# Kernel optimization log

Measured on AMD Instinct MI355X. Metric: run time of the kernel, lower is better.

Reference implementation:

```python
import jax, jax.numpy as jnp
import numpy as np

B, C, H, W = 8, 384, 32, 32
KEYS, HEADS, U = 16, 4, 1
VS = C // HEADS
N = H * W
BN_EPS = 1e-5


def setup_inputs() -> dict:
    key = jax.random.key(0)
    ks = jax.random.split(key, 8)
    x = jax.random.normal(ks[0], (B, C, H, W), dtype=jnp.float32)
    # 1x1 convs (spectral-normalized in torch; SN only rescales the weight,
    # so a plain weight matrix computes the same functional form)
    Wq = jax.random.normal(ks[1], (KEYS * HEADS, C), dtype=jnp.float32) * 0.02
    Wk = jax.random.normal(ks[2], (KEYS * U, C), dtype=jnp.float32) * 0.02
    Wv = jax.random.normal(ks[3], (VS * U, C), dtype=jnp.float32) * 0.02
    # BatchNorm affine params (torch code xavier-inits weight, zeros bias)
    gamma_q = jax.random.normal(ks[4], (KEYS * HEADS,), dtype=jnp.float32)
    beta_q = jnp.zeros((KEYS * HEADS,), dtype=jnp.float32)
    gamma_v = jax.random.normal(ks[5], (VS * U,), dtype=jnp.float32)
    beta_v = jnp.zeros((VS * U,), dtype=jnp.float32)
    pos_emb = jax.random.normal(ks[6], (N, N, KEYS, U), dtype=jnp.float32)
    return {"x": x, "Wq": Wq, "Wk": Wk, "Wv": Wv,
            "gamma_q": gamma_q, "beta_q": beta_q,
            "gamma_v": gamma_v, "beta_v": beta_v,
            "pos_emb": pos_emb}


def _bn(z, gamma, beta):
    # z: (B, Ch, N); BatchNorm2d in training mode: biased batch stats over (B, N)
    mean = jnp.mean(z, axis=(0, 2), keepdims=True)
    var = jnp.var(z, axis=(0, 2), keepdims=True)
    zn = (z - mean) * jax.lax.rsqrt(var + BN_EPS)
    return zn * gamma[None, :, None] + beta[None, :, None]


def reference(x, Wq, Wk, Wv, gamma_q, beta_q, gamma_v, beta_v, pos_emb):
    xf = x.reshape(B, C, N)                       # 1x1 conv == per-pixel matmul
    q = jnp.einsum('oc,bcn->bon', Wq, xf)         # (B, KEYS*HEADS, N)
    k = jnp.einsum('oc,bcn->bon', Wk, xf)         # (B, KEYS*U, N)
    v = jnp.einsum('oc,bcn->bon', Wv, xf)         # (B, VS*U, N)
    q = _bn(q, gamma_q, beta_q)
    v = _bn(v, gamma_v, beta_v)
    q = q.reshape(B, HEADS, KEYS, N)
    k = k.reshape(B, U, KEYS, N)
    v = v.reshape(B, U, VS, N)
    k = jax.nn.softmax(k, axis=-1)
    lambdac = jnp.einsum('bukm,buvm->bkv', k, v)          # content lambda
    Yc = jnp.einsum('bhkn,bkv->bhvn', q, lambdac)
    lambdap = jnp.einsum('nmku,buvm->bnkv', pos_emb, v)   # position lambda (B,N,K,V)
    Yp = jnp.einsum('bhkn,bnkv->bhvn', q, lambdap)
    Y = (Yc + Yp).reshape(B, C, H, W)
    return Y
```

## Files before the change

### kernel.cpp

```cpp
#include <hip/hip_runtime.h>

typedef __attribute__((ext_vector_type(8))) short short8;
typedef __attribute__((ext_vector_type(16))) float floatx16;
typedef __attribute__((ext_vector_type(4))) float floatx4;
typedef unsigned short ushort16_t;
typedef unsigned int uint32;

#define BB 8
#define CC 384
#define NPIX 1024
#define TOTCH 176
#define BN_EPS 1e-5f

__device__ __forceinline__ ushort16_t f2bf(float x) {
    uint32 u = __float_as_uint(x);
    u += 0x7FFFu + ((u >> 16) & 1u);
    return (ushort16_t)(u >> 16);
}
__device__ __forceinline__ uint32 pk2(float a, float b) {
    uint32 ua = __float_as_uint(a); ua += 0x7FFFu + ((ua >> 16) & 1u);
    uint32 ub = __float_as_uint(b); ub += 0x7FFFu + ((ub >> 16) & 1u);
    return (ua >> 16) | (ub & 0xFFFF0000u);
}
__device__ __forceinline__ void dma16(const ushort16_t* g, ushort16_t* l) {
    __builtin_amdgcn_global_load_lds(
        (const __attribute__((address_space(1))) uint32*)g,
        (__attribute__((address_space(3))) uint32*)l, 16, 0, 0);
}
__device__ __forceinline__ int div48(int x) {
    return (int)(((unsigned)x * 21846u) >> 20);
}


__global__ __launch_bounds__(256) void k_xt(const float* __restrict__ x,
    const float* __restrict__ Wq, const float* __restrict__ Wk,
    const float* __restrict__ Wv,
    ushort16_t* __restrict__ xbf, ushort16_t* __restrict__ wbf)
{
    int bx = blockIdx.x, t = threadIdx.x;
    if (bx < 256) {
        __shared__ __align__(16) ushort16_t T[32 * 392];
        int col0 = bx * 32;
        int b = col0 >> 10, nbase = col0 & 1023;
        const float* xb = x + (size_t)b * (CC * NPIX) + nbase;
        #pragma unroll
        for (int j = 0; j < 12; ++j) {
            int idx = t + 256 * j;
            int c = idx >> 3, ng = idx & 7;
            float4 f = *(const float4*)(xb + (size_t)c * NPIX + ng * 4);
            int n = ng * 4;
            T[(n + 0) * 392 + c] = f2bf(f.x);
            T[(n + 1) * 392 + c] = f2bf(f.y);
            T[(n + 2) * 392 + c] = f2bf(f.z);
            T[(n + 3) * 392 + c] = f2bf(f.w);
        }
        __syncthreads();
        #pragma unroll
        for (int j = 0; j < 6; ++j) {
            int task = t + 256 * j;
            int col = div48(task);
            int ch  = task - col * 48;
            uint4 w = *(const uint4*)&T[col * 392 + ch * 8];
            *(uint4*)&xbf[(size_t)(col0 + col) * CC + ch * 8] = w;
        }
    } else {
        #pragma unroll
        for (int jj = 0; jj < 9; ++jj) {
            int idx8 = ((bx - 256) * 9 + jj) * 256 + t;
            int row = div48(idx8);
            int g   = idx8 - row * 48;
            float4 f0, f1;
            if (row < 176) {
                const float* src;
                if (row < 64)       src = Wq + (size_t)row * CC;
                else if (row < 80)  src = Wk + (size_t)(row - 64) * CC;
                else                src = Wv + (size_t)(row - 80) * CC;
                f0 = *(const float4*)(src + g * 8);
                f1 = *(const float4*)(src + g * 8 + 4);
            } else {
                f0.x = f0.y = f0.z = f0.w = 0.f;
                f1 = f0;
            }
            uint4 w;
            w.x = pk2(f0.x, f0.y); w.y = pk2(f0.z, f0.w);
            w.z = pk2(f1.x, f1.y); w.w = pk2(f1.z, f1.w);
            *(uint4*)&wbf[(size_t)row * CC + g * 8] = w;
        }
    }
}

__global__ __launch_bounds__(256) void k_proj(const ushort16_t* __restrict__ xbf,
    const ushort16_t* __restrict__ wbf, float* __restrict__ qkv)
{
    int t = threadIdx.x;
    int wave = t >> 6, lane = t & 63;
    int ct = blockIdx.x * 4 + wave;
    int r0 = blockIdx.y * 16;
    int col = ct * 16 + (lane & 15);
    int kh  = lane >> 4;
    const ushort16_t* ap = wbf + (size_t)(r0 + (lane & 15)) * CC + kh * 8;
    const ushort16_t* bp = xbf + (size_t)col * CC + kh * 8;
    floatx4 acc = {0.f, 0.f, 0.f, 0.f};
    short8 a0 = *(const short8*)ap;
    short8 b0 = *(const short8*)bp;
    #pragma unroll
    for (int k = 1; k < 12; ++k) {
        short8 a1 = *(const short8*)(ap + k * 32);
        short8 b1 = *(const short8*)(bp + k * 32);
        acc = __builtin_amdgcn_mfma_f32_16x16x32_bf16(a0, b0, acc, 0, 0, 0);
        a0 = a1; b0 = b1;
    }
    acc = __builtin_amdgcn_mfma_f32_16x16x32_bf16(a0, b0, acc, 0, 0, 0);
    int b = col >> 10, n = col & 1023;
    #pragma unroll
    for (int r = 0; r < 4; ++r) {
        int ch = r0 + (lane >> 4) * 4 + r;
        qkv[((size_t)b * TOTCH + ch) * NPIX + n] = acc[r];
    }
}

__global__ __launch_bounds__(256) void k_bnsm(const float* __restrict__ qkv,
    const float* __restrict__ gq, const float* __restrict__ bq,
    const float* __restrict__ gv, const float* __restrict__ bv,
    float* __restrict__ sA, float* __restrict__ sB, float* __restrict__ ksm)
{
    int bx = blockIdx.x, tid = threadIdx.x;
    int wid = tid >> 6, lane = tid & 63;
    if (bx < 160) {
        int ch = bx;
        int row; float gamma, beta;
        if (ch < 64) { row = ch; gamma = gq[ch]; beta = bq[ch]; }
        else { int j = ch - 64; row = 80 + j; gamma = gv[j]; beta = bv[j]; }
        float s = 0.f, ss = 0.f;
        #pragma unroll
        for (int j = 0; j < 8; ++j) {
            int i4 = tid + 256 * j;
            int b = i4 >> 8, n4 = i4 & 255;
            float4 f = *(const float4*)(qkv + ((size_t)b * TOTCH + row) * NPIX
                                            + n4 * 4);
            s  += f.x + f.y + f.z + f.w;
            ss += f.x * f.x + f.y * f.y + f.z * f.z + f.w * f.w;
        }
        #pragma unroll
        for (int off = 32; off > 0; off >>= 1) {
            s  += __shfl_down(s, off);
            ss += __shfl_down(ss, off);
        }
        __shared__ float rs[4], rss[4];
        if (lane == 0) { rs[wid] = s; rss[wid] = ss; }
        __syncthreads();
        if (tid == 0) {
            float S  = rs[0] + rs[1] + rs[2] + rs[3];
            float SS = rss[0] + rss[1] + rss[2] + rss[3];
            float inv = 1.f / (BB * NPIX);
            float mean = S * inv;
            float var  = SS * inv - mean * mean;
            float a = gamma * rsqrtf(var + BN_EPS);
            sA[row] = a;
            sB[row] = beta - mean * a;
        }
    } else {
        int idx = bx - 160;
        int kc = idx & 15, b = idx >> 4;
        const float* rowp = qkv + ((size_t)b * TOTCH + 64 + kc) * NPIX;
        float4 v4 = *(const float4*)(rowp + tid * 4);
        float v[4] = {v4.x, v4.y, v4.z, v4.w};
        float mx = fmaxf(fmaxf(v[0], v[1]), fmaxf(v[2], v[3]));
        #pragma unroll
        for (int off = 32; off > 0; off >>= 1) mx = fmaxf(mx, __shfl_down(mx, off));
        __shared__ float sm[4], ssum[4];
        if (lane == 0) sm[wid] = mx;
        __syncthreads();
        mx = fmaxf(fmaxf(sm[0], sm[1]), fmaxf(sm[2], sm[3]));
        float e[4], s = 0.f;
        #pragma unroll
        for (int j = 0; j < 4; ++j) { e[j] = __expf(v[j] - mx); s += e[j]; }
        #pragma unroll
        for (int off = 32; off > 0; off >>= 1) s += __shfl_down(s, off);
        if (lane == 0) ssum[wid] = s;
        __syncthreads();
        float inv = 1.f / (ssum[0] + ssum[1] + ssum[2] + ssum[3]);
        float4 o;
        o.x = e[0] * inv; o.y = e[1] * inv; o.z = e[2] * inv; o.w = e[3] * inv;
        *(float4*)(ksm + ((size_t)b * 16 + kc) * NPIX + tid * 4) = o;
    }
}

__global__ __launch_bounds__(256) void k_packlc(const float* __restrict__ qkv,
    const float* __restrict__ sA, const float* __restrict__ sB,
    const float* __restrict__ ksm,
    ushort16_t* __restrict__ qt_g, ushort16_t* __restrict__ vt_g,
    ushort16_t* __restrict__ lc_g)
{
    int bx = blockIdx.x, t = threadIdx.x;
    if (bx < 128) {
        int bh = t & 31, nn = (t >> 5) & 7;
        int n = bx * 8 + nn;
        int b = bh >> 2, h = bh & 3;
        float vals[16];
        #pragma unroll
        for (int k = 0; k < 16; ++k) {
            int ch = h * 16 + k;
            vals[k] = qkv[((size_t)b * TOTCH + ch) * NPIX + n] * sA[ch] + sB[ch];
        }
        uint4 w0, w1;
        w0.x = pk2(vals[0], vals[1]);  w0.y = pk2(vals[2], vals[3]);
        w0.z = pk2(vals[4], vals[5]);  w0.w = pk2(vals[6], vals[7]);
        w1.x = pk2(vals[8], vals[9]);  w1.y = pk2(vals[10], vals[11]);
        w1.z = pk2(vals[12], vals[13]); w1.w = pk2(vals[14], vals[15]);
        *(uint4*)&qt_g[(size_t)n * 512 + bh * 8]       = w0;
        *(uint4*)&qt_g[(size_t)n * 512 + 256 + bh * 8] = w1;
    } else if (bx < 512) {
        int gi = (bx - 128) * 256 + t;
        int m8 = gi & 127;
        int vg = (gi >> 7) % 96;
        int b  = gi / (96 * 128);
        int m  = m8 * 8;
        int row = 80 + vg;
        float a = sA[row], bb = sB[row];
        const float* p = qkv + ((size_t)b * TOTCH + row) * NPIX + m;
        float4 f0 = *(const float4*)p;
        float4 f1 = *(const float4*)(p + 4);
        uint4 w;
        w.x = pk2(f0.x * a + bb, f0.y * a + bb);
        w.y = pk2(f0.z * a + bb, f0.w * a + bb);
        w.z = pk2(f1.x * a + bb, f1.y * a + bb);
        w.w = pk2(f1.z * a + bb, f1.w * a + bb);
        int mt = m >> 5, mq = (m >> 3) & 3;
        int vhh = vg / 48, vtt = (vg % 48) >> 4, vl = vg & 15;
        size_t idx = ((((size_t)b * 32 + mt) * 2 + vhh) * 3 + vtt) * 512
                   + mq * 128 + vl * 8;
        *(uint4*)&vt_g[idx] = w;
    } else {
        int gi = bx - 512;
        int v = gi % 96, b = gi / 96;
        int row = 80 + v;
        float a = sA[row], bb = sB[row];
        const float* vp = qkv + ((size_t)b * TOTCH + row) * NPIX;
        const float* kp = ksm + (size_t)b * 16 * NPIX;
        float acc[16];
        #pragma unroll
        for (int k = 0; k < 16; ++k) acc[k] = 0.f;
        for (int m = t; m < NPIX; m += 256) {
            float vv = vp[m] * a + bb;
            #pragma unroll
            for (int k = 0; k < 16; ++k) acc[k] += kp[k * NPIX + m] * vv;
        }
        #pragma unroll
        for (int k = 0; k < 16; ++k) {
            #pragma unroll
            for (int off = 32; off > 0; off >>= 1)
                acc[k] += __shfl_down(acc[k], off);
        }
        __shared__ float red[16][4];
        int wid = t >> 6, lane = t & 63;
        if (lane == 0) {
            #pragma unroll
            for (int k = 0; k < 16; ++k) red[k][wid] = acc[k];
        }
        __syncthreads();
        int vhh = v / 48, vtt = (v % 48) >> 4, vl = v & 15;
        size_t plane = ((size_t)(b * 2 + vhh) * 3 + vtt) * 512;
        if (t < 16) {
            int k = t;
            float val = red[k][0] + red[k][1] + red[k][2] + red[k][3];
            lc_g[plane + (k >> 3) * 128 + vl * 8 + (k & 7)] = f2bf(val);
        } else if (t < 18) {
            int mq = 2 + (t - 16);
            uint4 z; z.x = z.y = z.z = z.w = 0u;
            *(uint4*)&lc_g[plane + mq * 128 + vl * 8] = z;
        }
    }
}

__global__ __launch_bounds__(512, 2) void k_main(const float* __restrict__ pos,
    const ushort16_t* __restrict__ qt_g, const ushort16_t* __restrict__ vt_g,
    const ushort16_t* __restrict__ lc_g, float* __restrict__ out)
{
    __shared__ __align__(16) ushort16_t P_s[8192];
    __shared__ __align__(16) ushort16_t V_s[24576];
    __shared__ __align__(16) ushort16_t S_s[8192];
    int tid  = threadIdx.x;
    int lane = tid & 63;
    int wave = tid >> 6;
    int n0 = blockIdx.x * 8;
    int vh = blockIdx.y;

    int col1 = lane & 31, half = lane >> 5;
    int pb = col1 >> 2, ph = col1 & 3;
    int pplane = pb * 2 + (ph >> 1);
    int pf = pplane & 7;
    int pcb = ph & 1;
    int sm = tid & 31, snn = (tid >> 5) & 7, skh = (tid >> 8) & 1;
    int b2 = wave;

    short8 qfr = *(const short8*)(qt_g + (size_t)(n0 + wave) * 512
                                  + half * 256 + col1 * 8);

    floatx4 acc[2][3];
    #pragma unroll
    for (int hg = 0; hg < 2; ++hg)
        #pragma unroll
        for (int vt = 0; vt < 3; ++vt)
            acc[hg][vt] = floatx4{0.f, 0.f, 0.f, 0.f};

    const float* pbase = pos + ((size_t)(n0 + snn) * 1024 + sm) * 16 + skh * 8;

    {
        float4 f0 = *(const float4*)pbase;
        float4 f1 = *(const float4*)(pbase + 4);
        uint4 w;
        w.x = pk2(f0.x, f0.y); w.y = pk2(f0.z, f0.w);
        w.z = pk2(f1.x, f1.y); w.w = pk2(f1.z, f1.w);
        *(uint4*)&P_s[(snn * 2 + skh) * 256 + sm * 8] = w;
        const ushort16_t* src = vt_g + (size_t)(((b2 * 32) * 2 + vh) * 3) * 512;
        #pragma unroll
        for (int j = 0; j < 3; ++j)
            dma16(src + j * 512 + lane * 8, &V_s[b2 * 1536 + j * 512]);
    }
    __syncthreads();

    for (int it = 0; it < 32; ++it) {
        float4 pf0, pf1;
        if (it < 31) {
            const float* p = pbase + (size_t)(it + 1) * 32 * 16;
            pf0 = *(const float4*)p;
            pf1 = *(const float4*)(p + 4);
        }
        {
            short8 afr = *(const short8*)&P_s[(it & 1) * 4096
                + wave * 512 + half * 256 + col1 * 8];
            floatx16 d;
            #pragma unroll
            for (int i = 0; i < 16; ++i) d[i] = 0.f;
            d = __builtin_amdgcn_mfma_f32_32x32x16_bf16(afr, qfr, d, 0, 0, 0);
            int nx = wave ^ pf;
            #pragma unroll
            for (int q = 0; q < 4; ++q) {
                int c = q * 16 + pcb * 8 + nx;
                uint2 wv;
                wv.x = pk2(d[q * 4 + 0], d[q * 4 + 1]);
                wv.y = pk2(d[q * 4 + 2], d[q * 4 + 3]);
                *(uint2*)&S_s[pplane * 512 + c * 8 + half * 4] = wv;
            }
        }
        __syncthreads();
        if (it < 31) {
            const ushort16_t* src = vt_g
                + (size_t)(((b2 * 32 + it + 1) * 2 + vh) * 3) * 512;
            #pragma unroll
            for (int j = 0; j < 3; ++j)
                dma16(src + j * 512 + lane * 8,
                      &V_s[((it + 1) & 1) * 12288 + b2 * 1536 + j * 512]);
        }
        {
            int vb = (it & 1) * 12288;
            short8 av[3];
            #pragma unroll
            for (int vt = 0; vt < 3; ++vt)
                av[vt] = *(const short8*)&V_s[vb + b2 * 1536 + vt * 512 + lane * 8];
            #pragma unroll
            for (int hg = 0; hg < 2; ++hg) {
                int p2 = b2 * 2 + hg, f2 = p2 & 7;
                short8 bs = *(const short8*)&S_s[p2 * 512
                    + ((lane >> 4) * 16 + ((lane & 15) ^ f2)) * 8];
                #pragma unroll
                for (int vt = 0; vt < 3; ++vt)
                    acc[hg][vt] = __builtin_amdgcn_mfma_f32_16x16x32_bf16(
                        av[vt], bs, acc[hg][vt], 0, 0, 0);
            }
        }
        if (it < 31) {
            uint4 w;
            w.x = pk2(pf0.x, pf0.y); w.y = pk2(pf0.z, pf0.w);
            w.z = pk2(pf1.x, pf1.y); w.w = pk2(pf1.z, pf1.w);
            *(uint4*)&P_s[((it + 1) & 1) * 4096 + (snn * 2 + skh) * 256 + sm * 8] = w;
        }
        __syncthreads();
    }

    {
        const ushort16_t* src = lc_g + (size_t)((b2 * 2 + vh) * 3) * 512;
        #pragma unroll
        for (int j = 0; j < 3; ++j)
            dma16(src + j * 512 + lane * 8, &V_s[b2 * 1536 + j * 512]);
    }
    {
        int c = half * 16 + pcb * 8 + (wave ^ pf);
        *(short8*)&S_s[pplane * 512 + c * 8] = qfr;
        int zp = tid >> 5, zr = tid & 31;
        int zc = (2 + (zr >> 4)) * 16 + ((zr & 15) ^ (zp & 7));
        uint4 z; z.x = z.y = z.z = z.w = 0u;
        *(uint4*)&S_s[zp * 512 + zc * 8] = z;
    }
    __syncthreads();
    {
        short8 av[3];
        #pragma unroll
        for (int vt = 0; vt < 3; ++vt)
            av[vt] = *(const short8*)&V_s[b2 * 1536 + vt * 512 + lane * 8];
        #pragma unroll
        for (int hg = 0; hg < 2; ++hg) {
            int p2 = b2 * 2 + hg, f2 = p2 & 7;
            short8 bs = *(const short8*)&S_s[p2 * 512
                + ((lane >> 4) * 16 + ((lane & 15) ^ f2)) * 8];
            #pragma unroll
            for (int vt = 0; vt < 3; ++vt)
                acc[hg][vt] = __builtin_amdgcn_mfma_f32_16x16x32_bf16(
                    av[vt], bs, acc[hg][vt], 0, 0, 0);
        }
    }

    {
        int cn = lane & 15;
        int nloc = cn & 7;
        #pragma unroll
        for (int hg = 0; hg < 2; ++hg) {
            int h = hg * 2 + (cn >> 3);
            #pragma unroll
            for (int vt = 0; vt < 3; ++vt) {
                #pragma unroll
                for (int r = 0; r < 4; ++r) {
                    int v = vh * 48 + vt * 16 + (lane >> 4) * 4 + r;
                    out[(size_t)(b2 * 384 + h * 96 + v) * 1024 + n0 + nloc]
                        = acc[hg][vt][r];
                }
            }
        }
    }
}

extern "C" void kernel_launch(void* const* d_in, const int* in_sizes, int n_in,
                              void* d_out, int out_size, void* d_ws, size_t ws_size,
                              hipStream_t stream) {
    const float* x   = (const float*)d_in[0];
    const float* Wq  = (const float*)d_in[1];
    const float* Wk  = (const float*)d_in[2];
    const float* Wv  = (const float*)d_in[3];
    const float* gq  = (const float*)d_in[4];
    const float* bq  = (const float*)d_in[5];
    const float* gv  = (const float*)d_in[6];
    const float* bv  = (const float*)d_in[7];
    const float* pos = (const float*)d_in[8];
    float* out = (float*)d_out;
    float* ws  = (float*)d_ws;

    float* qkv = ws;
    float* sA  = ws + 1441792;
    float* sB  = ws + 1441968;
    float* ksm = ws + 1442144;
    ushort16_t* qt_g = (ushort16_t*)(ws + 1573216);
    ushort16_t* vt_g = (ushort16_t*)(ws + 1835360);
    ushort16_t* lc_g = (ushort16_t*)(ws + 2228576);
    ushort16_t* xbf  = (ushort16_t*)(ws + 2240864);
    ushort16_t* wbf  = (ushort16_t*)(ws + 3813728);

    k_xt<<<dim3(260), dim3(256), 0, stream>>>(x, Wq, Wk, Wv, xbf, wbf);
    k_proj<<<dim3(128, 11), dim3(256), 0, stream>>>(xbf, wbf, qkv);
    k_bnsm<<<dim3(288), dim3(256), 0, stream>>>(qkv, gq, bq, gv, bv, sA, sB, ksm);
    k_packlc<<<dim3(1280), dim3(256), 0, stream>>>(qkv, sA, sB, ksm,
                                                   qt_g, vt_g, lc_g);
    k_main<<<dim3(128, 2), dim3(512), 0, stream>>>(pos, qt_g, vt_g, lc_g, out);
}
```

Measured before the change: 184.8 us.

## Load position fragments directly into registers and double-buffer scores to drop a barrier

Each wave now loads its pos_emb rows straight into the MFMA A-operand layout and converts them to bf16 in registers. This removes the P_s shared-memory staging buffer along with its stores and loads. The score tile S_s is double-buffered, so the second __syncthreads in each of the 32 iterations can go, leaving one barrier per step. In exchange, each lane issues its own strided 32-byte global loads and the kernel holds extra prefetch registers, and shared-memory use stays about the same.

```diff
diff --git a/kernel.cpp b/kernel.cpp
--- a/kernel.cpp
+++ b/kernel.cpp
@@ -277,9 +277,8 @@
     const ushort16_t* __restrict__ qt_g, const ushort16_t* __restrict__ vt_g,
     const ushort16_t* __restrict__ lc_g, float* __restrict__ out)
 {
-    __shared__ __align__(16) ushort16_t P_s[8192];
-    __shared__ __align__(16) ushort16_t V_s[24576];
-    __shared__ __align__(16) ushort16_t S_s[8192];
+    __shared__ __align__(16) ushort16_t V_s[2][12288];
+    __shared__ __align__(16) ushort16_t S_s[2][8192];
     int tid  = threadIdx.x;
     int lane = tid & 63;
     int wave = tid >> 6;
@@ -291,7 +290,6 @@
     int pplane = pb * 2 + (ph >> 1);
     int pf = pplane & 7;
     int pcb = ph & 1;
-    int sm = tid & 31, snn = (tid >> 5) & 7, skh = (tid >> 8) & 1;
     int b2 = wave;
 
     short8 qfr = *(const short8*)(qt_g + (size_t)(n0 + wave) * 512
@@ -304,44 +302,44 @@
         for (int vt = 0; vt < 3; ++vt)
             acc[hg][vt] = floatx4{0.f, 0.f, 0.f, 0.f};
 
-    const float* pbase = pos + ((size_t)(n0 + snn) * 1024 + sm) * 16 + skh * 8;
-
+    floatx16 z16;
+    #pragma unroll
+    for (int i = 0; i < 16; ++i) z16[i] = 0.f;
+
+    const float* pA = pos + ((size_t)(n0 + wave) * 1024 + col1) * 16 + half * 8;
+
+    float4 a0 = *(const float4*)pA;
+    float4 a1 = *(const float4*)(pA + 4);
     {
-        float4 f0 = *(const float4*)pbase;
-        float4 f1 = *(const float4*)(pbase + 4);
-        uint4 w;
-        w.x = pk2(f0.x, f0.y); w.y = pk2(f0.z, f0.w);
-        w.z = pk2(f1.x, f1.y); w.w = pk2(f1.z, f1.w);
-        *(uint4*)&P_s[(snn * 2 + skh) * 256 + sm * 8] = w;
-        const ushort16_t* src = vt_g + (size_t)(((b2 * 32) * 2 + vh) * 3) * 512;
+        const ushort16_t* src = vt_g + (size_t)((b2 * 32 * 2 + vh) * 3) * 512;
         #pragma unroll
         for (int j = 0; j < 3; ++j)
-            dma16(src + j * 512 + lane * 8, &V_s[b2 * 1536 + j * 512]);
-    }
-    __syncthreads();
+            dma16(src + j * 512 + lane * 8, &V_s[0][b2 * 1536 + j * 512]);
+    }
 
     for (int it = 0; it < 32; ++it) {
-        float4 pf0, pf1;
+        float4 na0, na1;
         if (it < 31) {
-            const float* p = pbase + (size_t)(it + 1) * 32 * 16;
-            pf0 = *(const float4*)p;
-            pf1 = *(const float4*)(p + 4);
+            const float* p = pA + (size_t)(it + 1) * 512;
+            na0 = *(const float4*)p;
+            na1 = *(const float4*)(p + 4);
         }
         {
-            short8 afr = *(const short8*)&P_s[(it & 1) * 4096
-                + wave * 512 + half * 256 + col1 * 8];
-            floatx16 d;
-            #pragma unroll
-            for (int i = 0; i < 16; ++i) d[i] = 0.f;
-            d = __builtin_amdgcn_mfma_f32_32x32x16_bf16(afr, qfr, d, 0, 0, 0);
+            uint4 aw;
+            aw.x = pk2(a0.x, a0.y); aw.y = pk2(a0.z, a0.w);
+            aw.z = pk2(a1.x, a1.y); aw.w = pk2(a1.z, a1.w);
+            short8 afr = *(short8*)&aw;
+            floatx16 d = __builtin_amdgcn_mfma_f32_32x32x16_bf16(
+                afr, qfr, z16, 0, 0, 0);
             int nx = wave ^ pf;
+            ushort16_t* Sb = S_s[it & 1];
             #pragma unroll
             for (int q = 0; q < 4; ++q) {
                 int c = q * 16 + pcb * 8 + nx;
                 uint2 wv;
                 wv.x = pk2(d[q * 4 + 0], d[q * 4 + 1]);
                 wv.y = pk2(d[q * 4 + 2], d[q * 4 + 3]);
-                *(uint2*)&S_s[pplane * 512 + c * 8 + half * 4] = wv;
+                *(uint2*)&Sb[pplane * 512 + c * 8 + half * 4] = wv;
             }
         }
         __syncthreads();
@@ -351,18 +349,19 @@
             #pragma unroll
             for (int j = 0; j < 3; ++j)
                 dma16(src + j * 512 + lane * 8,
-                      &V_s[((it + 1) & 1) * 12288 + b2 * 1536 + j * 512]);
+                      &V_s[(it + 1) & 1][b2 * 1536 + j * 512]);
         }
         {
-            int vb = (it & 1) * 12288;
+            const ushort16_t* Vb = V_s[it & 1];
+            const ushort16_t* Sb = S_s[it & 1];
             short8 av[3];
             #pragma unroll
             for (int vt = 0; vt < 3; ++vt)
-                av[vt] = *(const short8*)&V_s[vb + b2 * 1536 + vt * 512 + lane * 8];
+                av[vt] = *(const short8*)&Vb[b2 * 1536 + vt * 512 + lane * 8];
             #pragma unroll
             for (int hg = 0; hg < 2; ++hg) {
                 int p2 = b2 * 2 + hg, f2 = p2 & 7;
-                short8 bs = *(const short8*)&S_s[p2 * 512
+                short8 bs = *(const short8*)&Sb[p2 * 512
                     + ((lane >> 4) * 16 + ((lane & 15) ^ f2)) * 8];
                 #pragma unroll
                 for (int vt = 0; vt < 3; ++vt)
@@ -370,39 +369,33 @@
                         av[vt], bs, acc[hg][vt], 0, 0, 0);
             }
         }
-        if (it < 31) {
-            uint4 w;
-            w.x = pk2(pf0.x, pf0.y); w.y = pk2(pf0.z, pf0.w);
-            w.z = pk2(pf1.x, pf1.y); w.w = pk2(pf1.z, pf1.w);
-            *(uint4*)&P_s[((it + 1) & 1) * 4096 + (snn * 2 + skh) * 256 + sm * 8] = w;
-        }
-        __syncthreads();
+        a0 = na0; a1 = na1;
     }
 
     {
         const ushort16_t* src = lc_g + (size_t)((b2 * 2 + vh) * 3) * 512;
         #pragma unroll
         for (int j = 0; j < 3; ++j)
-            dma16(src + j * 512 + lane * 8, &V_s[b2 * 1536 + j * 512]);
+            dma16(src + j * 512 + lane * 8, &V_s[0][b2 * 1536 + j * 512]);
     }
     {
         int c = half * 16 + pcb * 8 + (wave ^ pf);
-        *(short8*)&S_s[pplane * 512 + c * 8] = qfr;
+        *(short8*)&S_s[0][pplane * 512 + c * 8] = qfr;
         int zp = tid >> 5, zr = tid & 31;
         int zc = (2 + (zr >> 4)) * 16 + ((zr & 15) ^ (zp & 7));
         uint4 z; z.x = z.y = z.z = z.w = 0u;
-        *(uint4*)&S_s[zp * 512 + zc * 8] = z;
+        *(uint4*)&S_s[0][zp * 512 + zc * 8] = z;
     }
     __syncthreads();
     {
         short8 av[3];
         #pragma unroll
         for (int vt = 0; vt < 3; ++vt)
-            av[vt] = *(const short8*)&V_s[b2 * 1536 + vt * 512 + lane * 8];
+            av[vt] = *(const short8*)&V_s[0][b2 * 1536 + vt * 512 + lane * 8];
         #pragma unroll
         for (int hg = 0; hg < 2; ++hg) {
             int p2 = b2 * 2 + hg, f2 = p2 & 7;
-            short8 bs = *(const short8*)&S_s[p2 * 512
+            short8 bs = *(const short8*)&S_s[0][p2 * 512
                 + ((lane >> 4) * 16 + ((lane & 15) ^ f2)) * 8];
             #pragma unroll
             for (int vt = 0; vt < 3; ++vt)
```

Measured after the change: 184.5 us. About the same (-0.1%).
